# Kernel tuning notes

Hardware: AMD Instinct MI355X
Metric: run time of the kernel (lower is better)

## Reference

```python
import jax, jax.numpy as jnp
import numpy as np

SMOOTH = 0.5  # self.smooth from __init__

def setup_inputs() -> dict:
    key = jax.random.key(0)
    k1, k2, k3, k4, k5, k6 = jax.random.split(key, 6)
    N, E, F_IN, F_OUT = 100000, 3200000, 128, 128
    x = jax.random.normal(k1, (N, F_IN), dtype=jnp.float32)
    adj_rows = jax.random.randint(k2, (E,), 0, N, dtype=jnp.int32)
    adj_cols = jax.random.randint(k3, (E,), 0, N, dtype=jnp.int32)
    adj_vals = jax.random.uniform(k4, (E,), dtype=jnp.float32)
    stdv = 1.0 / np.sqrt(F_OUT)
    weight = jax.random.uniform(k5, (F_IN, F_OUT), dtype=jnp.float32, minval=-stdv, maxval=stdv)
    bias = jax.random.uniform(k6, (F_OUT,), dtype=jnp.float32, minval=-stdv, maxval=stdv)
    return {"x": x, "adj_rows": adj_rows, "adj_cols": adj_cols,
            "adj_vals": adj_vals, "weight": weight, "bias": bias}

def reference(x, adj_rows, adj_cols, adj_vals, weight, bias):
    # support = X @ W  (dense GEMM)
    support = x @ weight  # [N, F_out]
    n = x.shape[0]
    # adj @ support via edge-list gather + segment scatter-add
    gathered = support[adj_cols] * adj_vals[:, None]  # [E, F_out]
    agg = jax.ops.segment_sum(gathered, adj_rows, num_segments=n)  # [N, F_out]
    # ((I + smooth*adj) / (1 + smooth)) @ support + bias
    out = (support + SMOOTH * agg) / (1.0 + SMOOTH) + bias
    return out
```

## Files before the change

kernel.cpp:

```cpp
#include <hip/hip_runtime.h>
#include <hip/hip_fp16.h>

#define F 128
#define BM 64

#define SB_ROWS 256
#define SB_SHIFT 8
#define NBUCK_MAX 512
#define CAPS 8960
#define KREG 18
#define BIN_BLOCKS 512
#define NKEY 2048
#define COLG_SHIFT 14

#define LSTR 136

typedef _Float16 half8_t __attribute__((ext_vector_type(8)));
typedef float f32x4 __attribute__((ext_vector_type(4)));

__device__ inline __half2 h2of(unsigned u) {
    union { unsigned u; __half2 h; } x; x.u = u; return x.h;
}

__global__ __launch_bounds__(256) void gemm_kernel(
    const float* __restrict__ X, const float* __restrict__ W,
    _Float16* __restrict__ suph, int N)
{
    __shared__ _Float16 Wt[F * LSTR];
    __shared__ _Float16 Xh[BM * LSTR];

    const int t    = threadIdx.x;
    const int row0 = blockIdx.x * BM;

    for (int i = t; i < F * F; i += 256) {
        int k = i >> 7, c = i & 127;
        Wt[c * LSTR + k] = (_Float16)W[i];
    }
    for (int i = t; i < BM * (F / 4); i += 256) {
        int r = i >> 5, k4 = i & 31;
        int grow = row0 + r;
        float4 xv = make_float4(0.f, 0.f, 0.f, 0.f);
        if (grow < N) xv = ((const float4*)(X + (size_t)grow * F))[k4];
        _Float16* xp = &Xh[r * LSTR + k4 * 4];
        xp[0] = (_Float16)xv.x; xp[1] = (_Float16)xv.y;
        xp[2] = (_Float16)xv.z; xp[3] = (_Float16)xv.w;
    }
    __syncthreads();

    const int wv = t >> 6, lane = t & 63;
    const int fr = lane & 15, fq = lane >> 4;

    const _Float16* xa = Xh + (wv * 16 + fr) * LSTR + fq * 8;
    half8_t a0 = *(const half8_t*)(xa);
    half8_t a1 = *(const half8_t*)(xa + 32);
    half8_t a2 = *(const half8_t*)(xa + 64);
    half8_t a3 = *(const half8_t*)(xa + 96);

    #pragma unroll
    for (int tc = 0; tc < 8; ++tc) {
        const _Float16* wb = Wt + (tc * 16 + fr) * LSTR + fq * 8;
        f32x4 acc = {0.f, 0.f, 0.f, 0.f};
        acc = __builtin_amdgcn_mfma_f32_16x16x32_f16(a0, *(const half8_t*)(wb),      acc, 0, 0, 0);
        acc = __builtin_amdgcn_mfma_f32_16x16x32_f16(a1, *(const half8_t*)(wb + 32), acc, 0, 0, 0);
        acc = __builtin_amdgcn_mfma_f32_16x16x32_f16(a2, *(const half8_t*)(wb + 64), acc, 0, 0, 0);
        acc = __builtin_amdgcn_mfma_f32_16x16x32_f16(a3, *(const half8_t*)(wb + 96), acc, 0, 0, 0);

        const int col   = tc * 16 + fr;
        const int rbase = row0 + wv * 16 + fq * 4;
        #pragma unroll
        for (int r = 0; r < 4; ++r) {
            int row = rbase + r;
            if (row < N) suph[(size_t)row * F + col] = (_Float16)acc[r];
        }
    }
}

__global__ __launch_bounds__(256) void bin_kernel(
    const int* __restrict__ rows, const int* __restrict__ cols,
    const float* __restrict__ vals, int* __restrict__ cursor,
    int2* __restrict__ csr, int E, int nbuck)
{
    __shared__ int hist[NBUCK_MAX];
    __shared__ int base[NBUCK_MAX];

    const int t = threadIdx.x;
    int chunk = ((E + BIN_BLOCKS - 1) / BIN_BLOCKS + 3) & ~3;
    const int beg = blockIdx.x * chunk;
    const int end = min(beg + chunk, E);
    if (beg >= E) return;

    for (int b = t; b < nbuck; b += 256) hist[b] = 0;
    __syncthreads();

    int i = beg + t * 4;
    for (; i + 3 < end; i += 1024) {
        int4 r = *(const int4*)(rows + i);
        atomicAdd(&hist[r.x >> SB_SHIFT], 1);
        atomicAdd(&hist[r.y >> SB_SHIFT], 1);
        atomicAdd(&hist[r.z >> SB_SHIFT], 1);
        atomicAdd(&hist[r.w >> SB_SHIFT], 1);
    }
    for (; i < end; ++i) atomicAdd(&hist[rows[i] >> SB_SHIFT], 1);
    __syncthreads();

    for (int b = t; b < nbuck; b += 256) {
        int c = hist[b];
        base[b] = c ? atomicAdd(&cursor[b], c) : 0;
        hist[b] = 0;
    }
    __syncthreads();

    i = beg + t * 4;
    for (; i + 3 < end; i += 1024) {
        int4 r = *(const int4*)(rows + i);
        int4 c = *(const int4*)(cols + i);
        float4 v = *(const float4*)(vals + i);
        int rr[4] = {r.x, r.y, r.z, r.w};
        int cc[4] = {c.x, c.y, c.z, c.w};
        float vv[4] = {v.x, v.y, v.z, v.w};
        #pragma unroll
        for (int k = 0; k < 4; ++k) {
            int b  = rr[k] >> SB_SHIFT;
            int rl = rr[k] & (SB_ROWS - 1);
            int pos = base[b] + atomicAdd(&hist[b], 1);
            if (pos < CAPS)
                csr[(size_t)b * CAPS + pos] =
                    make_int2(cc[k] | (rl << 17), __float_as_int(vv[k]));
        }
    }
    for (; i < end; ++i) {
        int b  = rows[i] >> SB_SHIFT;
        int rl = rows[i] & (SB_ROWS - 1);
        int pos = base[b] + atomicAdd(&hist[b], 1);
        if (pos < CAPS)
            csr[(size_t)b * CAPS + pos] =
                make_int2(cols[i] | (rl << 17), __float_as_int(vals[i]));
    }
}

__global__ __launch_bounds__(512) void sortb_kernel(
    const int* __restrict__ cursor, int2* __restrict__ csr,
    int* __restrict__ offsB, int* __restrict__ offsE, int N)
{
    __shared__ int sc[NKEY];
    __shared__ int wsum[8];
    __shared__ int2 st[CAPS];

    const int b = blockIdx.x;
    const int t = threadIdx.x;
    const int cnt = min(cursor[b], CAPS);
    int2* reg = csr + (size_t)b * CAPS;

    int2 e[KREG];
    #pragma unroll
    for (int k = 0; k < KREG; ++k) {
        int idx = t + k * 512;
        e[k] = (idx < cnt) ? reg[idx] : make_int2(-1, 0);
    }

    for (int i = t; i < NKEY; i += 512) sc[i] = 0;
    __syncthreads();

    #pragma unroll
    for (int k = 0; k < KREG; ++k) {
        if (e[k].x >= 0) {
            unsigned p = (unsigned)e[k].x;
            int key = (int)(((p >> 17) << 3) | ((p >> COLG_SHIFT) & 7));
            atomicAdd(&sc[key], 1);
        }
    }
    __syncthreads();

    int c0 = sc[t * 4], c1 = sc[t * 4 + 1], c2 = sc[t * 4 + 2], c3 = sc[t * 4 + 3];
    int s = c0 + c1 + c2 + c3;
    int inc = s;
    const int lane = t & 63, w = t >> 6;
    #pragma unroll
    for (int d = 1; d < 64; d <<= 1) {
        int u = __shfl_up(inc, d, 64);
        if (lane >= d) inc += u;
    }
    if (lane == 63) wsum[w] = inc;
    __syncthreads();
    int wbase = 0;
    #pragma unroll
    for (int ww = 0; ww < 8; ++ww) if (ww < w) wbase += wsum[ww];
    int run = inc - s + wbase;
    sc[t * 4]     = run; run += c0;
    sc[t * 4 + 1] = run; run += c1;
    sc[t * 4 + 2] = run; run += c2;
    sc[t * 4 + 3] = run; run += c3;
    __syncthreads();

    if (t < SB_ROWS) {
        int row = b * SB_ROWS + t;
        if (row < N) {
            int gbase = b * CAPS;
            int x0 = sc[t * 8];
            int x1 = (t == SB_ROWS - 1) ? cnt : sc[t * 8 + 8];
            offsB[row] = gbase + x0;
            offsE[row] = gbase + x1;
        }
    }
    __syncthreads();

    #pragma unroll
    for (int k = 0; k < KREG; ++k) {
        if (e[k].x >= 0) {
            unsigned p = (unsigned)e[k].x;
            int key = (int)(((p >> 17) << 3) | ((p >> COLG_SHIFT) & 7));
            int pos = atomicAdd(&sc[key], 1);
            st[pos] = make_int2(e[k].x & 0x1FFFF, e[k].y);
        }
    }
    __syncthreads();

    for (int i = t; i < cnt; i += 512) reg[i] = st[i];
}

__global__ __launch_bounds__(256) void agg_kernel(
    const int* __restrict__ offsB, const int* __restrict__ offsE,
    const int2* __restrict__ csr, const __half* __restrict__ sup,
    const float* __restrict__ bias, float* __restrict__ out, int N)
{
    int wid  = (int)((blockIdx.x * 256 + threadIdx.x) >> 6);
    if (wid >= N) return;
    int lane = threadIdx.x & 63;
    int g  = lane >> 4;
    int sl = lane & 15;

    const int beg = offsB[wid];
    const int end = offsE[wid];
    const int len = end - beg;
    const int q   = (len + 3) >> 2;
    const int gb  = beg + g * q;
    const int ge  = min(gb + q, end);

    float acc[8];
    #pragma unroll
    for (int i = 0; i < 8; ++i) acc[i] = 0.f;

    int j = gb;
    for (; j + 3 < ge; j += 4) {
        int2 cv0 = csr[j];
        int2 cv1 = csr[j + 1];
        int2 cv2 = csr[j + 2];
        int2 cv3 = csr[j + 3];
        const uint4 s0 = *(const uint4*)(sup + (size_t)cv0.x * F + sl * 8);
        const uint4 s1 = *(const uint4*)(sup + (size_t)cv1.x * F + sl * 8);
        const uint4 s2 = *(const uint4*)(sup + (size_t)cv2.x * F + sl * 8);
        const uint4 s3 = *(const uint4*)(sup + (size_t)cv3.x * F + sl * 8);
        __half2 v0 = __float2half2_rn(__int_as_float(cv0.y));
        __half2 v1 = __float2half2_rn(__int_as_float(cv1.y));
        __half2 v2 = __float2half2_rn(__int_as_float(cv2.y));
        __half2 v3 = __float2half2_rn(__int_as_float(cv3.y));

        __half2 p0 = __hmul2(h2of(s0.x), v0);
        __half2 p1 = __hmul2(h2of(s0.y), v0);
        __half2 p2 = __hmul2(h2of(s0.z), v0);
        __half2 p3 = __hmul2(h2of(s0.w), v0);
        p0 = __hfma2(h2of(s1.x), v1, p0);
        p1 = __hfma2(h2of(s1.y), v1, p1);
        p2 = __hfma2(h2of(s1.z), v1, p2);
        p3 = __hfma2(h2of(s1.w), v1, p3);
        p0 = __hfma2(h2of(s2.x), v2, p0);
        p1 = __hfma2(h2of(s2.y), v2, p1);
        p2 = __hfma2(h2of(s2.z), v2, p2);
        p3 = __hfma2(h2of(s2.w), v2, p3);
        p0 = __hfma2(h2of(s3.x), v3, p0);
        p1 = __hfma2(h2of(s3.y), v3, p1);
        p2 = __hfma2(h2of(s3.z), v3, p2);
        p3 = __hfma2(h2of(s3.w), v3, p3);

        float2 f;
        f = __half22float2(p0); acc[0] += f.x; acc[1] += f.y;
        f = __half22float2(p1); acc[2] += f.x; acc[3] += f.y;
        f = __half22float2(p2); acc[4] += f.x; acc[5] += f.y;
        f = __half22float2(p3); acc[6] += f.x; acc[7] += f.y;
    }
    for (; j < ge; ++j) {
        int2 cv = csr[j];
        const uint4 s = *(const uint4*)(sup + (size_t)cv.x * F + sl * 8);
        __half2 v = __float2half2_rn(__int_as_float(cv.y));
        float2 f;
        f = __half22float2(__hmul2(h2of(s.x), v)); acc[0] += f.x; acc[1] += f.y;
        f = __half22float2(__hmul2(h2of(s.y), v)); acc[2] += f.x; acc[3] += f.y;
        f = __half22float2(__hmul2(h2of(s.z), v)); acc[4] += f.x; acc[5] += f.y;
        f = __half22float2(__hmul2(h2of(s.w), v)); acc[6] += f.x; acc[7] += f.y;
    }

    #pragma unroll
    for (int i = 0; i < 8; ++i) {
        acc[i] += __shfl_xor(acc[i], 16, 64);
        acc[i] += __shfl_xor(acc[i], 32, 64);
    }

    if (g == 0) {
        const uint4 s = *(const uint4*)(sup + (size_t)wid * F + sl * 8);
        float4 b0 = *(const float4*)(bias + sl * 8);
        float4 b1 = *(const float4*)(bias + sl * 8 + 4);
        const float inv = 1.0f / 1.5f, third = 1.0f / 3.0f;
        float2 sA = __half22float2(h2of(s.x));
        float2 sB = __half22float2(h2of(s.y));
        float2 sC = __half22float2(h2of(s.z));
        float2 sD = __half22float2(h2of(s.w));
        float4 o0, o1;
        o0.x = sA.x * inv + acc[0] * third + b0.x;
        o0.y = sA.y * inv + acc[1] * third + b0.y;
        o0.z = sB.x * inv + acc[2] * third + b0.z;
        o0.w = sB.y * inv + acc[3] * third + b0.w;
        o1.x = sC.x * inv + acc[4] * third + b1.x;
        o1.y = sC.y * inv + acc[5] * third + b1.y;
        o1.z = sD.x * inv + acc[6] * third + b1.z;
        o1.w = sD.y * inv + acc[7] * third + b1.w;
        float* op = out + (size_t)wid * F + sl * 8;
        *(float4*)(op)     = o0;
        *(float4*)(op + 4) = o1;
    }
}

extern "C" void kernel_launch(void* const* d_in, const int* in_sizes, int n_in,
                              void* d_out, int out_size, void* d_ws, size_t ws_size,
                              hipStream_t stream) {
    const float* x        = (const float*)d_in[0];
    const int*   adj_rows = (const int*)  d_in[1];
    const int*   adj_cols = (const int*)  d_in[2];
    const float* adj_vals = (const float*)d_in[3];
    const float* weight   = (const float*)d_in[4];
    const float* bias     = (const float*)d_in[5];

    const int N = in_sizes[0] / F;
    const int E = in_sizes[1];
    const int nbuck = (N + SB_ROWS - 1) / SB_ROWS;

    float* out = (float*)d_out;
    char*  ws  = (char*)d_ws;

    auto align = [](size_t v) { return (v + 255) & ~(size_t)255; };
    size_t off_sup    = 0;
    size_t sz_sup     = align((size_t)N * F * sizeof(_Float16));
    size_t off_csr    = off_sup + sz_sup;
    size_t sz_csr     = align((size_t)nbuck * CAPS * sizeof(int2));
    size_t off_offsB  = off_csr + sz_csr;
    size_t sz_offsB   = align((size_t)N * sizeof(int));
    size_t off_offsE  = off_offsB + sz_offsB;
    size_t sz_offsE   = align((size_t)N * sizeof(int));
    size_t off_cursor = off_offsE + sz_offsE;

    _Float16* suph = (_Float16*)(ws + off_sup);
    int2* csr    = (int2*)(ws + off_csr);
    int*  offsB  = (int*) (ws + off_offsB);
    int*  offsE  = (int*) (ws + off_offsE);
    int*  cursor = (int*) (ws + off_cursor);

    hipMemsetAsync(cursor, 0, (size_t)nbuck * sizeof(int), stream);

    gemm_kernel<<<(N + BM - 1) / BM, 256, 0, stream>>>(x, weight, suph, N);

    bin_kernel<<<BIN_BLOCKS, 256, 0, stream>>>(
        adj_rows, adj_cols, adj_vals, cursor, csr, E, nbuck);

    sortb_kernel<<<nbuck, 512, 0, stream>>>(cursor, csr, offsB, offsE, N);

    agg_kernel<<<(N + 3) / 4, 256, 0, stream>>>(
        offsB, offsE, csr, (const __half*)suph, bias, out, N);
}
```

Baseline: 201.5 us.

## Split binning into histogram, per-bucket scan, and deterministic placement kernels

Replaces the single bin kernel, which counted edges per bucket and then reserved space with global atomics on a shared cursor, with three passes. The passes write per-block histograms, run an exclusive scan per bucket across blocks, and place edges at precomputed offsets. This removes the global atomic contention and the memset, makes bucket layout deterministic, and doubles the block count to 1024. In exchange it adds two kernel launches, reads the row array twice, and moves extra count/base arrays through memory. The scan kernel assumes exactly 1024 blocks, two per thread.

```diff
diff --git a/kernel.cpp b/kernel.cpp
--- a/kernel.cpp
+++ b/kernel.cpp
@@ -9,7 +9,7 @@
 #define NBUCK_MAX 512
 #define CAPS 8960
 #define KREG 18
-#define BIN_BLOCKS 512
+#define HBLK 1024
 #define NKEY 2048
 #define COLG_SHIFT 14
 
@@ -75,42 +75,88 @@
     }
 }
 
-__global__ __launch_bounds__(256) void bin_kernel(
+__global__ __launch_bounds__(256) void hist_kernel(
+    const int* __restrict__ rows, int* __restrict__ counts, int E, int nbuck)
+{
+    __shared__ int hist[NBUCK_MAX];
+    const int t = threadIdx.x;
+    int chunk = ((E + HBLK - 1) / HBLK + 3) & ~3;
+    const int beg = blockIdx.x * chunk;
+    const int end = min(beg + chunk, E);
+
+    for (int b = t; b < nbuck; b += 256) hist[b] = 0;
+    __syncthreads();
+
+    if (beg < E) {
+        int i = beg + t * 4;
+        for (; i + 3 < end; i += 1024) {
+            int4 r = *(const int4*)(rows + i);
+            atomicAdd(&hist[r.x >> SB_SHIFT], 1);
+            atomicAdd(&hist[r.y >> SB_SHIFT], 1);
+            atomicAdd(&hist[r.z >> SB_SHIFT], 1);
+            atomicAdd(&hist[r.w >> SB_SHIFT], 1);
+        }
+        for (; i < end; ++i) atomicAdd(&hist[rows[i] >> SB_SHIFT], 1);
+    }
+    __syncthreads();
+
+    int* my = counts + (size_t)blockIdx.x * nbuck;
+    for (int b = t; b < nbuck; b += 256) my[b] = hist[b];
+}
+
+__global__ __launch_bounds__(512) void scan_kernel(
+    const int* __restrict__ counts, int* __restrict__ bases,
+    int* __restrict__ totals, int nbuck)
+{
+    __shared__ int wsum[8];
+    const int b = blockIdx.x;
+    const int t = threadIdx.x;
+    const int lane = t & 63, w = t >> 6;
+
+    int v0 = counts[(size_t)(2 * t)     * nbuck + b];
+    int v1 = counts[(size_t)(2 * t + 1) * nbuck + b];
+    int s = v0 + v1;
+    int inc = s;
+    #pragma unroll
+    for (int d = 1; d < 64; d <<= 1) {
+        int u = __shfl_up(inc, d, 64);
+        if (lane >= d) inc += u;
+    }
+    if (lane == 63) wsum[w] = inc;
+    __syncthreads();
+    int wbase = 0;
+    #pragma unroll
+    for (int ww = 0; ww < 8; ++ww) if (ww < w) wbase += wsum[ww];
+    int ex = inc - s + wbase;
+    bases[(size_t)(2 * t)     * nbuck + b] = ex;
+    bases[(size_t)(2 * t + 1) * nbuck + b] = ex + v0;
+    if (t == 0) {
+        int tot = 0;
+        #pragma unroll
+        for (int ww = 0; ww < 8; ++ww) tot += wsum[ww];
+        totals[b] = tot;
+    }
+}
+
+__global__ __launch_bounds__(256) void place_kernel(
     const int* __restrict__ rows, const int* __restrict__ cols,
-    const float* __restrict__ vals, int* __restrict__ cursor,
+    const float* __restrict__ vals, const int* __restrict__ bases,
     int2* __restrict__ csr, int E, int nbuck)
 {
-    __shared__ int hist[NBUCK_MAX];
     __shared__ int base[NBUCK_MAX];
+    __shared__ int lc[NBUCK_MAX];
 
     const int t = threadIdx.x;
-    int chunk = ((E + BIN_BLOCKS - 1) / BIN_BLOCKS + 3) & ~3;
+    int chunk = ((E + HBLK - 1) / HBLK + 3) & ~3;
     const int beg = blockIdx.x * chunk;
     const int end = min(beg + chunk, E);
     if (beg >= E) return;
 
-    for (int b = t; b < nbuck; b += 256) hist[b] = 0;
+    const int* my = bases + (size_t)blockIdx.x * nbuck;
+    for (int b = t; b < nbuck; b += 256) { base[b] = my[b]; lc[b] = 0; }
     __syncthreads();
 
     int i = beg + t * 4;
-    for (; i + 3 < end; i += 1024) {
-        int4 r = *(const int4*)(rows + i);
-        atomicAdd(&hist[r.x >> SB_SHIFT], 1);
-        atomicAdd(&hist[r.y >> SB_SHIFT], 1);
-        atomicAdd(&hist[r.z >> SB_SHIFT], 1);
-        atomicAdd(&hist[r.w >> SB_SHIFT], 1);
-    }
-    for (; i < end; ++i) atomicAdd(&hist[rows[i] >> SB_SHIFT], 1);
-    __syncthreads();
-
-    for (int b = t; b < nbuck; b += 256) {
-        int c = hist[b];
-        base[b] = c ? atomicAdd(&cursor[b], c) : 0;
-        hist[b] = 0;
-    }
-    __syncthreads();
-
-    i = beg + t * 4;
     for (; i + 3 < end; i += 1024) {
         int4 r = *(const int4*)(rows + i);
         int4 c = *(const int4*)(cols + i);
@@ -122,7 +168,7 @@
         for (int k = 0; k < 4; ++k) {
             int b  = rr[k] >> SB_SHIFT;
             int rl = rr[k] & (SB_ROWS - 1);
-            int pos = base[b] + atomicAdd(&hist[b], 1);
+            int pos = base[b] + atomicAdd(&lc[b], 1);
             if (pos < CAPS)
                 csr[(size_t)b * CAPS + pos] =
                     make_int2(cc[k] | (rl << 17), __float_as_int(vv[k]));
@@ -131,7 +177,7 @@
     for (; i < end; ++i) {
         int b  = rows[i] >> SB_SHIFT;
         int rl = rows[i] & (SB_ROWS - 1);
-        int pos = base[b] + atomicAdd(&hist[b], 1);
+        int pos = base[b] + atomicAdd(&lc[b], 1);
         if (pos < CAPS)
             csr[(size_t)b * CAPS + pos] =
                 make_int2(cols[i] | (rl << 17), __float_as_int(vals[i]));
@@ -139,7 +185,7 @@
 }
 
 __global__ __launch_bounds__(512) void sortb_kernel(
-    const int* __restrict__ cursor, int2* __restrict__ csr,
+    const int* __restrict__ totals, int2* __restrict__ csr,
     int* __restrict__ offsB, int* __restrict__ offsE, int N)
 {
     __shared__ int sc[NKEY];
@@ -148,7 +194,7 @@
 
     const int b = blockIdx.x;
     const int t = threadIdx.x;
-    const int cnt = min(cursor[b], CAPS);
+    const int cnt = min(totals[b], CAPS);
     int2* reg = csr + (size_t)b * CAPS;
 
     int2 e[KREG];
@@ -345,22 +391,30 @@
     size_t sz_offsB   = align((size_t)N * sizeof(int));
     size_t off_offsE  = off_offsB + sz_offsB;
     size_t sz_offsE   = align((size_t)N * sizeof(int));
-    size_t off_cursor = off_offsE + sz_offsE;
+    size_t off_counts = off_offsE + sz_offsE;
+    size_t sz_counts  = align((size_t)HBLK * nbuck * sizeof(int));
+    size_t off_bases  = off_counts + sz_counts;
+    size_t sz_bases   = align((size_t)HBLK * nbuck * sizeof(int));
+    size_t off_totals = off_bases + sz_bases;
 
     _Float16* suph = (_Float16*)(ws + off_sup);
     int2* csr    = (int2*)(ws + off_csr);
     int*  offsB  = (int*) (ws + off_offsB);
     int*  offsE  = (int*) (ws + off_offsE);
-    int*  cursor = (int*) (ws + off_cursor);
-
-    hipMemsetAsync(cursor, 0, (size_t)nbuck * sizeof(int), stream);
+    int*  counts = (int*) (ws + off_counts);
+    int*  bases  = (int*) (ws + off_bases);
+    int*  totals = (int*) (ws + off_totals);
 
     gemm_kernel<<<(N + BM - 1) / BM, 256, 0, stream>>>(x, weight, suph, N);
 
-    bin_kernel<<<BIN_BLOCKS, 256, 0, stream>>>(
-        adj_rows, adj_cols, adj_vals, cursor, csr, E, nbuck);
-
-    sortb_kernel<<<nbuck, 512, 0, stream>>>(cursor, csr, offsB, offsE, N);
+    hist_kernel<<<HBLK, 256, 0, stream>>>(adj_rows, counts, E, nbuck);
+
+    scan_kernel<<<nbuck, 512, 0, stream>>>(counts, bases, totals, nbuck);
+
+    place_kernel<<<HBLK, 256, 0, stream>>>(
+        adj_rows, adj_cols, adj_vals, bases, csr, E, nbuck);
+
+    sortb_kernel<<<nbuck, 512, 0, stream>>>(totals, csr, offsB, offsE, N);
 
     agg_kernel<<<(N + 3) / 4, 256, 0, stream>>>(
         offsB, offsE, csr, (const __half*)suph, bias, out, N);
```

New measurement: 197.9 us. About the same (-1.7%).
